# Kernel tuning notes

Measured on AMD Instinct MI355X. Metric: run time of the kernel, lower is better.

Reference implementation:

```python
import jax, jax.numpy as jnp
import numpy as np

B, D, H, W = 32, 256, 32, 32
K = 2048


def setup_inputs() -> dict:
    key = jax.random.key(0)
    k1, k2 = jax.random.split(key)
    x = jax.random.normal(k1, (B, D, H, W), dtype=jnp.float32)
    # nn.Parameter uniform_(-0.5, 0.5), shape [embedding_dim, num_embeddings]
    embedding_table = jax.random.uniform(k2, (D, K), dtype=jnp.float32, minval=-0.5, maxval=0.5)
    return {"x": x, "embedding_table": embedding_table}


def _l2norm(v, axis):
    return v / jnp.maximum(jnp.linalg.norm(v, axis=axis, keepdims=True), 1e-12)


def reference(x, embedding_table):
    b, d, h, w = x.shape
    k = embedding_table.shape[1]
    # [B,C,H,W] -> [B,H,W,C] -> [N,D]
    flat_x = jnp.transpose(x, (0, 2, 3, 1)).reshape(-1, d)

    # l2-normalized vectors used only for distance computation
    fx = _l2norm(flat_x, axis=1)
    et = _l2norm(embedding_table, axis=0)

    # ||fx||^2 - 2 fx.et + ||et||^2  -> [N,K]
    distances = (
        jnp.sum(fx * fx, axis=1, keepdims=True)
        - 2.0 * (fx @ et)
        + jnp.sum(et * et, axis=0, keepdims=True)
    )
    encoding_indices = jnp.argmin(distances, axis=1)  # [N]

    # gather from UNnormalized table (matches original), -> [B,H,W,D] -> [B,D,H,W]
    quantized = embedding_table.T[encoding_indices].reshape(b, h, w, d)
    quantized_x = jnp.transpose(quantized, (0, 3, 1, 2))

    dictionary_loss = jnp.mean((jax.lax.stop_gradient(x) - quantized_x) ** 2)
    commitment_loss = jnp.mean((x - jax.lax.stop_gradient(quantized_x)) ** 2)

    # straight-through estimator
    quantized_x = x + jax.lax.stop_gradient(quantized_x - x)

    counts = jnp.bincount(encoding_indices, length=k)
    probs = counts / jnp.sum(counts)
    entropy_loss = jnp.sum(probs * jnp.log(probs + 1e-10))

    return (
        quantized_x,
        dictionary_loss,
        commitment_loss,
        entropy_loss,
        encoding_indices.reshape(b, -1),
    )
```

## Files before the change

kernel.cpp:

```cpp
#include <hip/hip_runtime.h>
#include <hip/hip_bf16.h>
#include <hip/hip_fp16.h>
#include <math.h>

#define KN 2048
#define DN 256
#define NN 32768
#define HW 1024
#define XSTR 260

typedef _Float16 half8 __attribute__((ext_vector_type(8)));
typedef float floatx4 __attribute__((ext_vector_type(4)));


__global__ __launch_bounds__(256) void k_norm(const float* __restrict__ E,
                                              double* __restrict__ normsq) {
  const int c = ((blockIdx.x & 7) << 8) + threadIdx.x;
  const int ds = blockIdx.x >> 3;
  const float* p = E + (size_t)(ds * 32) * KN + c;
  double s = 0.0;
#pragma unroll 8
  for (int d = 0; d < 32; ++d) {
    double v = (double)p[(size_t)d * KN];
    s = fma(v, v, s);
  }
  atomicAdd(&normsq[c], s);
}

__global__ __launch_bounds__(256) void k_convE(const float* __restrict__ E,
                                               const double* __restrict__ normsq,
                                               _Float16* __restrict__ Et) {
  const int c = ((blockIdx.x & 7) << 8) + threadIdx.x;
  const int dg = blockIdx.x >> 3;
  const int kh = dg >> 2, lg = dg & 3;
  const int nc = c >> 7, w = (c >> 5) & 3, nf = (c >> 4) & 1, col16 = c & 15;
  const int t = nc * 8 + kh;
  double nr = sqrt(normsq[c]);
  if (nr < 1e-12) nr = 1e-12;
  const double inv = 1.0 / nr;
  const size_t base =
      (size_t)t * 8192 + w * 2048 + nf * 512 + (lg * 16 + col16) * 8;
  half8 hv, lv;
#pragma unroll
  for (int j = 0; j < 8; ++j) {
    float v = (float)((double)E[(size_t)(dg * 8 + j) * KN + c] * inv);
    _Float16 h = (_Float16)v;
    hv[j] = h;
    lv[j] = (_Float16)((v - (float)h) * 4096.0f);
  }
  *(half8*)(Et + base) = hv;
  *(half8*)(Et + base + 1024) = lv;
}

__device__ __forceinline__ void gload_lds16(const void* g, void* l) {
  __builtin_amdgcn_global_load_lds(
      (const __attribute__((address_space(1))) unsigned int*)g,
      (__attribute__((address_space(3))) unsigned int*)l, 16, 0, 0);
}

#define STAGE(t, buf)                                                        \
  {                                                                          \
    const size_t gb_ = (size_t)(t) * 8192;                                   \
    const int lb_ = (buf) * 16384;                                           \
    _Pragma("unroll") for (int q_ = 0; q_ < 4; ++q_)                         \
        gload_lds16(Et + gb_ + q_ * 2048 + tid * 8,                          \
                    lds + lb_ + q_ * 4096 + tid * 16);                       \
  }

#define ITER(nc, ncp, kh, WAITOP, DO_STAGE)                                  \
  {                                                                          \
    asm volatile(WAITOP ::: "memory");                                       \
    __builtin_amdgcn_s_barrier();                                            \
    __builtin_amdgcn_sched_barrier(0);                                       \
    const int t_ = (nc)*8 + (kh);                                            \
    if (DO_STAGE) { STAGE(t_ + 2, ((2 * (ncp) + (kh) + 2) % 3)); }           \
    const char* wb_ = lds + ((2 * (ncp) + (kh)) % 3) * 16384 + w * 4096;     \
    half8 bh_[2], bl_[2];                                                    \
    bh_[0] = *(const half8*)(wb_ + lane * 16);                               \
    bh_[1] = *(const half8*)(wb_ + 1024 + lane * 16);                        \
    bl_[0] = *(const half8*)(wb_ + 2048 + lane * 16);                        \
    bl_[1] = *(const half8*)(wb_ + 3072 + lane * 16);                        \
    __builtin_amdgcn_s_setprio(1);                                           \
    _Pragma("unroll") for (int mf_ = 0; mf_ < 2; ++mf_)                      \
        _Pragma("unroll") for (int nf_ = 0; nf_ < 2; ++nf_) {                \
      accm[mf_][nf_] = __builtin_amdgcn_mfma_f32_16x16x32_f16(               \
          ah[mf_][(kh)], bh_[nf_], accm[mf_][nf_], 0, 0, 0);                 \
      accc[mf_][nf_] = __builtin_amdgcn_mfma_f32_16x16x32_f16(               \
          ah[mf_][(kh)], bl_[nf_], accc[mf_][nf_], 0, 0, 0);                 \
      accc[mf_][nf_] = __builtin_amdgcn_mfma_f32_16x16x32_f16(               \
          al[mf_][(kh)], bh_[nf_], accc[mf_][nf_], 0, 0, 0);                 \
    }                                                                        \
    __builtin_amdgcn_s_setprio(0);                                           \
  }

#define ZEROACC                                                              \
  {                                                                          \
    _Pragma("unroll") for (int mf_ = 0; mf_ < 2; ++mf_)                      \
        _Pragma("unroll") for (int nf_ = 0; nf_ < 2; ++nf_) {                \
      accm[mf_][nf_] = (floatx4)0.0f;                                        \
      accc[mf_][nf_] = (floatx4)0.0f;                                        \
    }                                                                        \
  }

#define EPILOGUE(nc)                                                         \
  {                                                                          \
    _Pragma("unroll") for (int nf_ = 0; nf_ < 2; ++nf_) {                    \
      const int c_ = (nc)*128 + w * 32 + nf_ * 16 + c16;                     \
      _Pragma("unroll") for (int mf_ = 0; mf_ < 2; ++mf_)                    \
          _Pragma("unroll") for (int r_ = 0; r_ < 4; ++r_) {                 \
        const double s_ = (double)accm[mf_][nf_][r_] +                       \
                          (double)accc[mf_][nf_][r_] * (1.0 / 4096.0);       \
        if (s_ > best[mf_][r_]) { best[mf_][r_] = s_; bidx[mf_][r_] = c_; }  \
      }                                                                      \
    }                                                                        \
  }

#define W4 "s_waitcnt vmcnt(4)"
#define W0 "s_waitcnt vmcnt(0)"

__global__ __launch_bounds__(256, 2) void k_score(
    const float* __restrict__ x, const _Float16* __restrict__ Et,
    int* __restrict__ idx_ws, float* __restrict__ fidx_out,
    int* __restrict__ counts) {
  __shared__ __align__(16) char lds[49152];
  const int tid = threadIdx.x;
  const int lane = tid & 63;
  const int w = tid >> 6;
  const int lg = lane >> 4;
  const int c16 = lane & 15;
  const int rowbase = blockIdx.x * 32;

  {
    float* xs = (float*)lds;
    const int r = tid & 31;
    const int d0 = tid >> 5;
    const int n = rowbase + r;
    const float* xb = x + (size_t)(n >> 10) * (DN * HW) + (n & 1023);
#pragma unroll
    for (int d = d0; d < DN; d += 8)
      xs[r * XSTR + d] = xb[(size_t)d * HW];
  }
  __syncthreads();

  half8 ah[2][8], al[2][8];
  {
    const float* xs = (const float*)lds;
#pragma unroll
    for (int mf = 0; mf < 2; ++mf)
#pragma unroll
      for (int kh = 0; kh < 8; ++kh) {
        const float* p = xs + (mf * 16 + c16) * XSTR + kh * 32 + lg * 8;
        half8 h, l;
#pragma unroll
        for (int i = 0; i < 8; ++i) {
          float v = p[i];
          _Float16 hh = (_Float16)v;
          h[i] = hh;
          l[i] = (_Float16)((v - (float)hh) * 4096.0f);
        }
        ah[mf][kh] = h;
        al[mf][kh] = l;
      }
  }
  __syncthreads();

  double best[2][4];
  int bidx[2][4];
#pragma unroll
  for (int mf = 0; mf < 2; ++mf)
#pragma unroll
    for (int r = 0; r < 4; ++r) { best[mf][r] = -1e300; bidx[mf][r] = 0; }

  floatx4 accm[2][2], accc[2][2];

  STAGE(0, 0);
  STAGE(1, 1);

  for (int nc3 = 0; nc3 < 5; ++nc3) {
#pragma unroll
    for (int ncp = 0; ncp < 3; ++ncp) {
      const int nc = nc3 * 3 + ncp;
      ZEROACC;
      ITER(nc, ncp, 0, W4, 1);
      ITER(nc, ncp, 1, W4, 1);
      ITER(nc, ncp, 2, W4, 1);
      ITER(nc, ncp, 3, W4, 1);
      ITER(nc, ncp, 4, W4, 1);
      ITER(nc, ncp, 5, W4, 1);
      ITER(nc, ncp, 6, W4, 1);
      ITER(nc, ncp, 7, W4, 1);
      EPILOGUE(nc);
    }
  }
  ZEROACC;
  ITER(15, 0, 0, W4, 1);
  ITER(15, 0, 1, W4, 1);
  ITER(15, 0, 2, W4, 1);
  ITER(15, 0, 3, W4, 1);
  ITER(15, 0, 4, W4, 1);
  ITER(15, 0, 5, W4, 1);
  ITER(15, 0, 6, W4, 0);
  ITER(15, 0, 7, W0, 0);
  EPILOGUE(15);

  __syncthreads();
  double* redD = (double*)lds;
  int* redI = (int*)(lds + 16384);
  const int ent = w * 16 + c16;
#pragma unroll
  for (int mf = 0; mf < 2; ++mf)
#pragma unroll
    for (int r = 0; r < 4; ++r) {
      const int row = mf * 16 + lg * 4 + r;
      redD[row * 64 + ent] = best[mf][r];
      redI[row * 64 + ent] = bidx[mf][r];
    }
  __syncthreads();
  if (tid < 32) {
    double bd = -1e300;
    int bi = 1 << 30;
    for (int e = 0; e < 64; ++e) {
      double dv = redD[tid * 64 + e];
      int iv = redI[tid * 64 + e];
      if (dv > bd || (dv == bd && iv < bi)) { bd = dv; bi = iv; }
    }
    const int n = rowbase + tid;
    idx_ws[n] = bi;
    fidx_out[n] = (float)bi;
    atomicAdd(&counts[bi], 1);
  }
}

__global__ __launch_bounds__(256) void k_quant(const float* __restrict__ x,
                                               const float* __restrict__ E,
                                               const int* __restrict__ idx,
                                               float* __restrict__ out,
                                               float* __restrict__ lossparts) {
  const int T = blockIdx.x * 256 + threadIdx.x;
  const int w4 = T & 7;
  int rest = T >> 3;
  const int h = rest & 31;
  rest >>= 5;
  const int d = rest & 255;
  const int b = rest >> 8;
  const int n = b * 1024 + h * 32 + w4 * 4;
  const int4 iv = *(const int4*)(idx + n);
  const size_t xoff = ((size_t)(b * 256 + d) << 10) + h * 32 + w4 * 4;
  const float4 xv = *(const float4*)(x + xoff);
  const float* Er = E + (size_t)d * KN;
  float4 q;
  q.x = Er[iv.x];
  q.y = Er[iv.y];
  q.z = Er[iv.z];
  q.w = Er[iv.w];
  *(float4*)(out + xoff) = q;
  const float dx = xv.x - q.x, dy = xv.y - q.y, dz = xv.z - q.z, dw = xv.w - q.w;
  float s = dx * dx + dy * dy + dz * dz + dw * dw;
#pragma unroll
  for (int off = 32; off > 0; off >>= 1) s += __shfl_down(s, off, 64);
  __shared__ float red[4];
  const int lane = threadIdx.x & 63, wv = threadIdx.x >> 6;
  if (lane == 0) red[wv] = s;
  __syncthreads();
  if (threadIdx.x == 0)
    atomicAdd(&lossparts[blockIdx.x & 255], red[0] + red[1] + red[2] + red[3]);
}

__global__ __launch_bounds__(256) void k_final(const int* __restrict__ counts,
                                               const float* __restrict__ lossparts,
                                               float* __restrict__ out) {
  __shared__ double redE[256];
  __shared__ double redL[256];
  const int tid = threadIdx.x;
  double t = 0.0;
  for (int u = tid; u < KN; u += 256) {
    float p = (float)counts[u] * (1.0f / 32768.0f);
    t += (double)(p * logf(p + 1e-10f));
  }
  redE[tid] = t;
  redL[tid] = (double)lossparts[tid];
  __syncthreads();
  for (int s2 = 128; s2 > 0; s2 >>= 1) {
    if (tid < s2) {
      redE[tid] += redE[tid + s2];
      redL[tid] += redL[tid + s2];
    }
    __syncthreads();
  }
  if (tid == 0) {
    float L = (float)(redL[0] * (1.0 / 8388608.0));
    out[8388608] = L;
    out[8388609] = L;
    out[8388610] = (float)redE[0];
  }
}

extern "C" void kernel_launch(void* const* d_in, const int* in_sizes, int n_in,
                              void* d_out, int out_size, void* d_ws, size_t ws_size,
                              hipStream_t stream) {
  const float* x = (const float*)d_in[0];
  const float* E = (const float*)d_in[1];
  float* out = (float*)d_out;
  char* ws = (char*)d_ws;
  int* counts = (int*)ws;
  float* lossparts = (float*)(ws + 8192);
  double* normsq = (double*)(ws + 16384);
  int* idx = (int*)(ws + 32768);
  _Float16* Et = (_Float16*)(ws + 163840);

  hipMemsetAsync(ws, 0, 32768, stream);
  k_norm<<<64, 256, 0, stream>>>(E, normsq);
  k_convE<<<256, 256, 0, stream>>>(E, normsq, Et);
  k_score<<<NN / 32, 256, 0, stream>>>(x, Et, idx, out + 8388611, counts);
  k_quant<<<(NN * DN / 4) / 256, 256, 0, stream>>>(x, E, idx, out, lossparts);
  k_final<<<1, 256, 0, stream>>>(counts, lossparts, out);
}
```

Baseline: 219.1 us.

## Load codebook fragments directly into registers, dropping the LDS staging pipeline

Replaces the triple-buffered global->LDS async staging with per-wave direct global loads of the B fragments into a register double buffer. This removes the per-step barriers and LDS traffic, and lets the LDS footprint shrink. Each wave reads only its own slice, so LDS sharing was not needed. The risk is exposed global or L2 latency, since only one tile of prefetch distance is covered by register double-buffering. It also pins waves_per_eu to 2.

```diff
diff --git a/kernel.cpp b/kernel.cpp
--- a/kernel.cpp
+++ b/kernel.cpp
@@ -52,45 +52,40 @@
   *(half8*)(Et + base + 1024) = lv;
 }
 
-__device__ __forceinline__ void gload_lds16(const void* g, void* l) {
-  __builtin_amdgcn_global_load_lds(
-      (const __attribute__((address_space(1))) unsigned int*)g,
-      (__attribute__((address_space(3))) unsigned int*)l, 16, 0, 0);
-}
-
-#define STAGE(t, buf)                                                        \
-  {                                                                          \
-    const size_t gb_ = (size_t)(t) * 8192;                                   \
-    const int lb_ = (buf) * 16384;                                           \
-    _Pragma("unroll") for (int q_ = 0; q_ < 4; ++q_)                         \
-        gload_lds16(Et + gb_ + q_ * 2048 + tid * 8,                          \
-                    lds + lb_ + q_ * 4096 + tid * 16);                       \
-  }
-
-#define ITER(nc, ncp, kh, WAITOP, DO_STAGE)                                  \
-  {                                                                          \
-    asm volatile(WAITOP ::: "memory");                                       \
-    __builtin_amdgcn_s_barrier();                                            \
-    __builtin_amdgcn_sched_barrier(0);                                       \
-    const int t_ = (nc)*8 + (kh);                                            \
-    if (DO_STAGE) { STAGE(t_ + 2, ((2 * (ncp) + (kh) + 2) % 3)); }           \
-    const char* wb_ = lds + ((2 * (ncp) + (kh)) % 3) * 16384 + w * 4096;     \
-    half8 bh_[2], bl_[2];                                                    \
-    bh_[0] = *(const half8*)(wb_ + lane * 16);                               \
-    bh_[1] = *(const half8*)(wb_ + 1024 + lane * 16);                        \
-    bl_[0] = *(const half8*)(wb_ + 2048 + lane * 16);                        \
-    bl_[1] = *(const half8*)(wb_ + 3072 + lane * 16);                        \
+
+#define LOADB(buf, t)                                                        \
+  {                                                                          \
+    const _Float16* p_ = bbase + (size_t)(t) * 8192;                         \
+    buf[0] = *(const half8*)(p_);                                            \
+    buf[1] = *(const half8*)(p_ + 512);                                      \
+    buf[2] = *(const half8*)(p_ + 1024);                                     \
+    buf[3] = *(const half8*)(p_ + 1536);                                     \
+  }
+
+#define COMP(kh, buf)                                                        \
+  {                                                                          \
     __builtin_amdgcn_s_setprio(1);                                           \
-    _Pragma("unroll") for (int mf_ = 0; mf_ < 2; ++mf_)                      \
-        _Pragma("unroll") for (int nf_ = 0; nf_ < 2; ++nf_) {                \
-      accm[mf_][nf_] = __builtin_amdgcn_mfma_f32_16x16x32_f16(               \
-          ah[mf_][(kh)], bh_[nf_], accm[mf_][nf_], 0, 0, 0);                 \
-      accc[mf_][nf_] = __builtin_amdgcn_mfma_f32_16x16x32_f16(               \
-          ah[mf_][(kh)], bl_[nf_], accc[mf_][nf_], 0, 0, 0);                 \
-      accc[mf_][nf_] = __builtin_amdgcn_mfma_f32_16x16x32_f16(               \
-          al[mf_][(kh)], bh_[nf_], accc[mf_][nf_], 0, 0, 0);                 \
+    _Pragma("unroll") for (int mf_ = 0; mf_ < 2; ++mf_) {                    \
+      accm[mf_][0] = __builtin_amdgcn_mfma_f32_16x16x32_f16(                 \
+          ah[mf_][(kh)], buf[0], accm[mf_][0], 0, 0, 0);                     \
+      accm[mf_][1] = __builtin_amdgcn_mfma_f32_16x16x32_f16(                 \
+          ah[mf_][(kh)], buf[1], accm[mf_][1], 0, 0, 0);                     \
+      accc[mf_][0] = __builtin_amdgcn_mfma_f32_16x16x32_f16(                 \
+          ah[mf_][(kh)], buf[2], accc[mf_][0], 0, 0, 0);                     \
+      accc[mf_][1] = __builtin_amdgcn_mfma_f32_16x16x32_f16(                 \
+          ah[mf_][(kh)], buf[3], accc[mf_][1], 0, 0, 0);                     \
+      accc[mf_][0] = __builtin_amdgcn_mfma_f32_16x16x32_f16(                 \
+          al[mf_][(kh)], buf[0], accc[mf_][0], 0, 0, 0);                     \
+      accc[mf_][1] = __builtin_amdgcn_mfma_f32_16x16x32_f16(                 \
+          al[mf_][(kh)], buf[1], accc[mf_][1], 0, 0, 0);                     \
     }                                                                        \
     __builtin_amdgcn_s_setprio(0);                                           \
+  }
+
+#define ITERX(kh, BUF, DOLOAD, tp2)                                          \
+  {                                                                          \
+    COMP(kh, BUF);                                                           \
+    if (DOLOAD) { LOADB(BUF, tp2); }                                         \
   }
 
 #define ZEROACC                                                              \
@@ -115,14 +110,12 @@
     }                                                                        \
   }
 
-#define W4 "s_waitcnt vmcnt(4)"
-#define W0 "s_waitcnt vmcnt(0)"
-
-__global__ __launch_bounds__(256, 2) void k_score(
+__global__ __launch_bounds__(256, 2)
+__attribute__((amdgpu_waves_per_eu(2, 2))) void k_score(
     const float* __restrict__ x, const _Float16* __restrict__ Et,
     int* __restrict__ idx_ws, float* __restrict__ fidx_out,
     int* __restrict__ counts) {
-  __shared__ __align__(16) char lds[49152];
+  __shared__ __align__(16) char lds[33280];
   const int tid = threadIdx.x;
   const int lane = tid & 63;
   const int w = tid >> 6;
@@ -162,7 +155,6 @@
         al[mf][kh] = l;
       }
   }
-  __syncthreads();
 
   double best[2][4];
   int bidx[2][4];
@@ -172,35 +164,34 @@
     for (int r = 0; r < 4; ++r) { best[mf][r] = -1e300; bidx[mf][r] = 0; }
 
   floatx4 accm[2][2], accc[2][2];
-
-  STAGE(0, 0);
-  STAGE(1, 1);
-
-  for (int nc3 = 0; nc3 < 5; ++nc3) {
-#pragma unroll
-    for (int ncp = 0; ncp < 3; ++ncp) {
-      const int nc = nc3 * 3 + ncp;
-      ZEROACC;
-      ITER(nc, ncp, 0, W4, 1);
-      ITER(nc, ncp, 1, W4, 1);
-      ITER(nc, ncp, 2, W4, 1);
-      ITER(nc, ncp, 3, W4, 1);
-      ITER(nc, ncp, 4, W4, 1);
-      ITER(nc, ncp, 5, W4, 1);
-      ITER(nc, ncp, 6, W4, 1);
-      ITER(nc, ncp, 7, W4, 1);
-      EPILOGUE(nc);
-    }
+  half8 b0[4], b1[4];
+  const _Float16* bbase = Et + w * 2048 + lane * 8;
+
+  LOADB(b0, 0);
+  LOADB(b1, 1);
+
+  for (int nc = 0; nc < 15; ++nc) {
+    const int t0 = nc * 8;
+    ZEROACC;
+    ITERX(0, b0, 1, t0 + 2);
+    ITERX(1, b1, 1, t0 + 3);
+    ITERX(2, b0, 1, t0 + 4);
+    ITERX(3, b1, 1, t0 + 5);
+    ITERX(4, b0, 1, t0 + 6);
+    ITERX(5, b1, 1, t0 + 7);
+    ITERX(6, b0, 1, t0 + 8);
+    ITERX(7, b1, 1, t0 + 9);
+    EPILOGUE(nc);
   }
   ZEROACC;
-  ITER(15, 0, 0, W4, 1);
-  ITER(15, 0, 1, W4, 1);
-  ITER(15, 0, 2, W4, 1);
-  ITER(15, 0, 3, W4, 1);
-  ITER(15, 0, 4, W4, 1);
-  ITER(15, 0, 5, W4, 1);
-  ITER(15, 0, 6, W4, 0);
-  ITER(15, 0, 7, W0, 0);
+  ITERX(0, b0, 1, 122);
+  ITERX(1, b1, 1, 123);
+  ITERX(2, b0, 1, 124);
+  ITERX(3, b1, 1, 125);
+  ITERX(4, b0, 1, 126);
+  ITERX(5, b1, 1, 127);
+  ITERX(6, b0, 0, 0);
+  ITERX(7, b1, 0, 0);
   EPILOGUE(15);
 
   __syncthreads();
```

Measured after the change: 209.6 us. 4.4% less time.
